# Performance work log

Measured on AMD Instinct MI355X. Metric: run time of the kernel, lower is better.

The kernel has to match this reference:

```python
import jax, jax.numpy as jnp
import numpy as np

B, S, D, H = 2, 2048, 512, 8
DH = D // H


def layer_norm(x, w, b, eps=1e-5):
    mu = x.mean(-1, keepdims=True)
    var = x.var(-1, keepdims=True)  # biased, matches nn.LayerNorm
    return (x - mu) / jnp.sqrt(var + eps) * w + b


def map_norm(qk, eps=1e-5):
    # torch.var default is unbiased (ddof=1)
    mu = qk.mean(-1, keepdims=True)
    var = qk.var(-1, ddof=1, keepdims=True)
    return (qk - mu) / jnp.sqrt(var + eps)


def sinmax(x):
    s = 1.0 + jnp.sin(10.0 * x)
    return s / s.sum(-1, keepdims=True)


def setup_inputs() -> dict:
    key = jax.random.key(0)
    ks = jax.random.split(key, 8)
    sc = 0.02
    return {
        "x": jax.random.normal(ks[0], (B, S, D), jnp.float32),
        "norm_w": jnp.ones((D,), jnp.float32),
        "norm_b": jnp.zeros((D,), jnp.float32),
        "qvk_w": jax.random.normal(ks[1], (D, 3 * D), jnp.float32) * sc,
        "qvk_b": jnp.zeros((3 * D,), jnp.float32),
        "concat_w": jax.random.normal(ks[2], (D, D), jnp.float32) * sc,
        "concat_b": jnp.zeros((D,), jnp.float32),
        "mlp_norm_w": jnp.ones((D,), jnp.float32),
        "mlp_norm_b": jnp.zeros((D,), jnp.float32),
        "mlp1_w": jax.random.normal(ks[3], (D, 2 * D), jnp.float32) * sc,
        "mlp1_b": jnp.zeros((2 * D,), jnp.float32),
        "mlp2_w": jax.random.normal(ks[4], (2 * D, D), jnp.float32) * sc,
        "mlp2_b": jnp.zeros((D,), jnp.float32),
    }


def reference(x, norm_w, norm_b, qvk_w, qvk_b, concat_w, concat_b,
              mlp_norm_w, mlp_norm_b, mlp1_w, mlp1_b, mlp2_w, mlp2_b):
    res = x
    xn = layer_norm(x, norm_w, norm_b)
    qvk = jax.nn.relu(xn @ qvk_w + qvk_b)                      # [B,S,3D]
    Q, K, V = qvk[..., :D], qvk[..., D:2 * D], qvk[..., 2 * D:]
    # contiguous d_per_head chunks per head == reshape to [B,S,H,DH]
    q = Q.reshape(B, S, H, DH).transpose(0, 2, 1, 3)           # [B,H,S,DH]
    k = K.reshape(B, S, H, DH).transpose(0, 2, 1, 3)
    v = V.reshape(B, S, H, DH).transpose(0, 2, 1, 3)
    qk = jnp.einsum('bhqd,bhkd->bhqk', q, k)                   # [B,H,S,S]
    qk = map_norm(qk)                                          # norm_ variant
    scores = sinmax(qk / np.sqrt(DH))                          # sinmax variant
    hv = jnp.einsum('bhqk,bhkd->bhqd', scores, v)
    attout = hv.transpose(0, 2, 1, 3).reshape(B, S, D)
    attout = attout @ concat_w + concat_b + res
    res_mlp = attout
    a = layer_norm(attout, mlp_norm_w, mlp_norm_b)
    h = jax.nn.gelu(a @ mlp1_w + mlp1_b, approximate=False)
    mlpout = h @ mlp2_w + mlp2_b
    return (mlpout + res_mlp, scores)
```

## Files before the change

### kernel.cpp

```cpp
#include <hip/hip_runtime.h>

#define Bb_ 2
#define S_ 2048
#define D_ 512
#define H_ 8
#define DH_ 64

typedef __attribute__((ext_vector_type(8))) __bf16 bf16x8;
typedef __attribute__((ext_vector_type(4))) __bf16 bf16x4;
typedef __attribute__((ext_vector_type(2))) __bf16 bf16x2;
typedef __attribute__((ext_vector_type(4))) float f32x4;
typedef __attribute__((ext_vector_type(8))) short short8;
typedef __attribute__((ext_vector_type(4))) unsigned u32x4;
typedef __attribute__((ext_vector_type(2))) unsigned u32x2;

__device__ __forceinline__ void gload_lds16(const void* g, void* l) {
  __builtin_amdgcn_global_load_lds(
      (const __attribute__((address_space(1))) unsigned int*)g,
      (__attribute__((address_space(3))) unsigned int*)l, 16, 0, 0);
}

__global__ __launch_bounds__(256) void wtrans_tile(
    const float* __restrict__ qvk_w, const float* __restrict__ concat_w,
    const float* __restrict__ mlp1_w, const float* __restrict__ mlp2_w,
    __bf16* __restrict__ qvk_wT, __bf16* __restrict__ concat_wT,
    __bf16* __restrict__ mlp1_wT, __bf16* __restrict__ mlp2_wT) {
  __shared__ __align__(16) __bf16 tl[64 * 72];
  int b = blockIdx.x;
  const float* w;
  __bf16* wt;
  int K, N, rel, TN;
  if (b < 192)      { w = qvk_w;    wt = qvk_wT;    K = 512;  N = 1536; rel = b;       TN = 24; }
  else if (b < 256) { w = concat_w; wt = concat_wT; K = 512;  N = 512;  rel = b - 192; TN = 8;  }
  else if (b < 384) { w = mlp1_w;   wt = mlp1_wT;   K = 512;  N = 1024; rel = b - 256; TN = 16; }
  else              { w = mlp2_w;   wt = mlp2_wT;   K = 1024; N = 512;  rel = b - 384; TN = 8;  }
  int tk = rel / TN, tn = rel % TN;
  int k0 = tk * 64, n0 = tn * 64;
  int t = threadIdx.x;
#pragma unroll
  for (int i = 0; i < 4; i++) {
    int idx = i * 256 + t;
    int kk = idx >> 4, c4 = idx & 15;
    float4 v = *reinterpret_cast<const float4*>(w + (long)(k0 + kk) * N + n0 + c4 * 4);
    int nb = c4 * 4;
    tl[(nb + 0) * 72 + kk] = (__bf16)v.x;
    tl[(nb + 1) * 72 + kk] = (__bf16)v.y;
    tl[(nb + 2) * 72 + kk] = (__bf16)v.z;
    tl[(nb + 3) * 72 + kk] = (__bf16)v.w;
  }
  __syncthreads();
#pragma unroll
  for (int i = 0; i < 2; i++) {
    int idx = i * 256 + t;
    int nn = idx >> 3, kc = idx & 7;
    bf16x8 vv = *reinterpret_cast<const bf16x8*>(&tl[nn * 72 + kc * 8]);
    *reinterpret_cast<bf16x8*>(wt + (long)(n0 + nn) * K + k0 + kc * 8) = vv;
  }
}

__global__ __launch_bounds__(256) void ln_kernel(const float* __restrict__ x,
                                                 const float* __restrict__ w,
                                                 const float* __restrict__ b,
                                                 __bf16* __restrict__ out) {
  long row = blockIdx.x;
  const float* xr = x + row * 512;
  int t = threadIdx.x;
  float2 v = *reinterpret_cast<const float2*>(xr + t * 2);
  float s = v.x + v.y;
  float sq = v.x * v.x + v.y * v.y;
#pragma unroll
  for (int m = 1; m < 64; m <<= 1) {
    s += __shfl_xor(s, m);
    sq += __shfl_xor(sq, m);
  }
  __shared__ float red[8];
  int wid = t >> 6;
  if ((t & 63) == 0) { red[wid] = s; red[wid + 4] = sq; }
  __syncthreads();
  s = red[0] + red[1] + red[2] + red[3];
  sq = red[4] + red[5] + red[6] + red[7];
  float mu = s * (1.f / 512.f);
  float var = sq * (1.f / 512.f) - mu * mu;
  float rs = rsqrtf(var + 1e-5f);
  int c = t * 2;
  float o0 = (v.x - mu) * rs * w[c] + b[c];
  float o1 = (v.y - mu) * rs * w[c + 1] + b[c + 1];
  bf16x2 ov;
  ov[0] = (__bf16)o0;
  ov[1] = (__bf16)o1;
  *reinterpret_cast<bf16x2*>(out + row * 512 + c) = ov;
}

template <int ACT, int OUTMODE, bool HASRES, int BM>
__global__ __launch_bounds__(256) void gemm_kernel(
    const __bf16* __restrict__ A, const __bf16* __restrict__ Bt,
    const float* __restrict__ bias, const float* __restrict__ res,
    float* __restrict__ outF, __bf16* __restrict__ outB,
    __bf16* __restrict__ outK, __bf16* __restrict__ outVt,
    int lda, int ldb, int ldc, int K) {
  __shared__ __align__(16) __bf16 smem[BM * 64 + 128 * 64];
  __bf16* As = smem;
  __bf16* Bs = smem + BM * 64;
  int t = threadIdx.x, lane = t & 63, wid = t >> 6;
  const __bf16* Ab = A + (long)blockIdx.y * BM * lda;
  const __bf16* Bb = Bt + (long)blockIdx.x * 128 * ldb;

  constexpr int WM = (BM == 128) ? 2 : 1;
  constexpr int FN = (BM == 128) ? 4 : 2;
  int wr = (WM == 2) ? (wid >> 1) : 0;
  int wc = (WM == 2) ? (wid & 1) : wid;
  int kq = lane >> 4;

  f32x4 acc[4][FN];
#pragma unroll
  for (int i = 0; i < 4; i++)
#pragma unroll
    for (int j = 0; j < FN; j++) acc[i][j] = (f32x4){0.f, 0.f, 0.f, 0.f};

  for (int k0 = 0; k0 < K; k0 += 64) {
    __syncthreads();
#pragma unroll
    for (int j = 0; j < BM / 32; j++) {
      int ci = wid * (BM * 2) + j * 64 + lane;
      int row = ci >> 3, c = ci & 7, sc = c ^ (row & 7);
      gload_lds16(Ab + (long)row * lda + k0 + sc * 8, &As[(wid * (BM * 2) + j * 64) * 8]);
    }
#pragma unroll
    for (int j = 0; j < 4; j++) {
      int ci = wid * 256 + j * 64 + lane;
      int row = ci >> 3, c = ci & 7, sc = c ^ (row & 7);
      gload_lds16(Bb + (long)row * ldb + k0 + sc * 8, &Bs[(wid * 256 + j * 64) * 8]);
    }
    __syncthreads();
#pragma unroll
    for (int ks = 0; ks < 2; ks++) {
      bf16x8 af[4], bfr[FN];
#pragma unroll
      for (int fm = 0; fm < 4; fm++) {
        int r = wr * 64 + fm * 16 + (lane & 15);
        int c = (ks * 4 + kq) ^ (r & 7);
        af[fm] = *reinterpret_cast<const bf16x8*>(&As[r * 64 + c * 8]);
      }
#pragma unroll
      for (int fn = 0; fn < FN; fn++) {
        int r = wc * (16 * FN) + fn * 16 + (lane & 15);
        int c = (ks * 4 + kq) ^ (r & 7);
        bfr[fn] = *reinterpret_cast<const bf16x8*>(&Bs[r * 64 + c * 8]);
      }
#pragma unroll
      for (int fm = 0; fm < 4; fm++)
#pragma unroll
        for (int fn = 0; fn < FN; fn++)
          acc[fm][fn] = __builtin_amdgcn_mfma_f32_16x16x32_bf16(af[fm], bfr[fn],
                                                                acc[fm][fn], 0, 0, 0);
    }
  }

  if constexpr (OUTMODE == 2) {
    __syncthreads();
    char* Cb = reinterpret_cast<char*>(smem);
#pragma unroll
    for (int fm = 0; fm < 4; fm++)
#pragma unroll
      for (int fn = 0; fn < FN; fn++) {
        int c = wc * 64 + fn * 16 + (lane & 15);
        int gcol = blockIdx.x * 128 + c;
        float bv = bias[gcol];
#pragma unroll
        for (int r4 = 0; r4 < 4; r4++) {
          int r = wr * 64 + fm * 16 + kq * 4 + r4;
          float v = fmaxf(acc[fm][fn][r4] + bv, 0.f);
          *reinterpret_cast<__bf16*>(Cb + r * 256 + (((c >> 3) ^ (r & 7)) << 4) +
                                     ((c & 7) << 1)) = (__bf16)v;
        }
      }
    __syncthreads();
    long bbq = (blockIdx.y * 128) >> 11;
    int srow0 = (blockIdx.y * 128) & 2047;
    if (blockIdx.x < 8) {
      int r = t >> 1, half = t & 1;
      int gcol = blockIdx.x * 128 + half * 64;
      __bf16* dst;
      if (gcol < 512)
        dst = outB + ((bbq * 8 + (gcol >> 6)) * 2048 + srow0 + r) * 64;
      else
        dst = outK + ((bbq * 8 + ((gcol - 512) >> 6)) * 2048 + srow0 + r) * 64;
      const char* srcrow = Cb + r * 256;
#pragma unroll
      for (int j = 0; j < 8; j++) {
        bf16x8 vv = *reinterpret_cast<const bf16x8*>(
            srcrow + ((((half * 8 + j) ^ (r & 7))) << 4));
        *reinterpret_cast<bf16x8*>(dst + j * 8) = vv;
      }
    } else {
      int d = t & 63, seg = t >> 6;
      int srow = srow0 + seg * 32;
#pragma unroll
      for (int h2 = 0; h2 < 2; h2++) {
        int c = h2 * 64 + d;
        int h = (blockIdx.x * 128 - 1024 + h2 * 64) >> 6;
        __bf16* dst = outVt + (bbq * 8 + h) * 131072 + (srow >> 5) * 2048 + d * 32;
        bf16x8 wv8[4];
#pragma unroll
        for (int i = 0; i < 32; i++) {
          int r = seg * 32 + i;
          __bf16 val = *reinterpret_cast<const __bf16*>(
              Cb + r * 256 + (((c >> 3) ^ (r & 7)) << 4) + ((c & 7) << 1));
          wv8[i >> 3][i & 7] = val;
        }
#pragma unroll
        for (int i4 = 0; i4 < 4; i4++)
          *reinterpret_cast<bf16x8*>(dst + i4 * 8) = wv8[i4];
      }
    }
    return;
  } else {
    long gr0 = (long)blockIdx.y * BM + wr * 64;
    long gc0 = (long)blockIdx.x * 128 + wc * (16 * FN);
#pragma unroll
    for (int fm = 0; fm < 4; fm++)
#pragma unroll
      for (int fn = 0; fn < FN; fn++) {
        int col = (int)gc0 + fn * 16 + (lane & 15);
        long rbase = gr0 + fm * 16 + kq * 4;
        float bv = bias ? bias[col] : 0.f;
#pragma unroll
        for (int r4 = 0; r4 < 4; r4++) {
          long grow = rbase + r4;
          float v = acc[fm][fn][r4] + bv;
          if (HASRES) v += res[grow * ldc + col];
          if (ACT == 1) v = fmaxf(v, 0.f);
          if (ACT == 2) v = 0.5f * v * (1.f + erff(v * 0.70710678118f));
          if (OUTMODE == 0) {
            outF[grow * ldc + col] = v;
          } else {
            outB[grow * ldc + col] = (__bf16)v;
          }
        }
      }
  }
}

__global__ __launch_bounds__(256) void gram_kernel(const __bf16* __restrict__ Kh,
                                                   float* __restrict__ gpart,
                                                   float* __restrict__ kpart) {
  int head = blockIdx.x >> 5, chunk = blockIdx.x & 31;
  __shared__ __align__(16) __bf16 kl[64 * 64];
  int t = threadIdx.x;
  const __bf16* src = Kh + ((long)head * 2048 + chunk * 64) * 64;
#pragma unroll
  for (int i = 0; i < 2; i++) {
    int e = (i * 256 + t) * 8;
    *reinterpret_cast<short8*>(&kl[e]) = *reinterpret_cast<const short8*>(&src[e]);
  }
  __syncthreads();
  int d1 = t & 63, g = t >> 6;
  float acc[16];
#pragma unroll
  for (int i = 0; i < 16; i++) acc[i] = 0.f;
  float kb = 0.f;
  for (int r = 0; r < 64; r++) {
    float k1 = (float)kl[r * 64 + d1];
    kb += k1;
    bf16x8 a = *reinterpret_cast<const bf16x8*>(&kl[r * 64 + g * 16]);
    bf16x8 b = *reinterpret_cast<const bf16x8*>(&kl[r * 64 + g * 16 + 8]);
#pragma unroll
    for (int i = 0; i < 8; i++) acc[i] += k1 * (float)a[i];
#pragma unroll
    for (int i = 0; i < 8; i++) acc[8 + i] += k1 * (float)b[i];
  }
  float* gp = gpart + ((long)chunk * 16 + head) * 4096 + d1 * 64 + g * 16;
#pragma unroll
  for (int i = 0; i < 16; i++) gp[i] = acc[i];
  if (g == 0) kpart[(chunk * 16 + head) * 64 + d1] = kb;
}

__global__ __launch_bounds__(256) void greduce_kernel(const float* __restrict__ gpart,
                                                      const float* __restrict__ kpart,
                                                      float* __restrict__ G,
                                                      float* __restrict__ kbar) {
  int idx = blockIdx.x * 256 + threadIdx.x;
  if (idx < 65536) {
    int head = idx >> 12, e = idx & 4095;
    float s = 0.f;
#pragma unroll 4
    for (int c = 0; c < 32; c++) s += gpart[((long)c * 16 + head) * 4096 + e];
    G[idx] = s;
  } else if (idx < 66560) {
    int k = idx - 65536;
    int head = k >> 6, d = k & 63;
    float s = 0.f;
#pragma unroll 4
    for (int c = 0; c < 32; c++) s += kpart[(c * 16 + head) * 64 + d];
    kbar[k] = s * (1.f / 2048.f);
  }
}

__global__ __launch_bounds__(256, 4) void stats_kernel(const __bf16* __restrict__ Qh,
                                                       const float* __restrict__ G,
                                                       const float* __restrict__ kbar,
                                                       float2* __restrict__ stats) {
  int head = blockIdx.x >> 5, sub = blockIdx.x & 31;
  __shared__ float Gl[4096];
  __shared__ float kbl[64];
  __shared__ __align__(16) float qlf[64 * 68];
  int t = threadIdx.x;
  const float* Gsrc = G + head * 4096;
#pragma unroll
  for (int i = 0; i < 4; i++) {
    int e = (i * 256 + t) * 4;
    *reinterpret_cast<float4*>(&Gl[e]) = *reinterpret_cast<const float4*>(&Gsrc[e]);
  }
  if (t < 16)
    *reinterpret_cast<float4*>(&kbl[t * 4]) =
        *reinterpret_cast<const float4*>(&kbar[head * 64 + t * 4]);
  const __bf16* qsrc = Qh + ((long)head * 2048 + sub * 64) * 64;
#pragma unroll
  for (int i = 0; i < 2; i++) {
    int e = (i * 256 + t) * 8;
    bf16x8 v = *reinterpret_cast<const bf16x8*>(&qsrc[e]);
    int row = e >> 6, col = e & 63;
    float* dst = &qlf[row * 68 + col];
#pragma unroll
    for (int j = 0; j < 8; j++) dst[j] = (float)v[j];
  }
  __syncthreads();
  int qrow = t >> 2, qt = t & 3;
  const float* qr = &qlf[qrow * 68];
  float mup = 0.f, s2p = 0.f;
#pragma unroll
  for (int i = 0; i < 16; i++) {
    int d1 = qt * 16 + i;
    const float* Gr = &Gl[d1 * 64];
    float acc = 0.f;
#pragma unroll
    for (int j = 0; j < 64; j++) acc += Gr[j] * qr[j];
    float q1 = qr[d1];
    s2p += q1 * acc;
    mup += q1 * kbl[d1];
  }
  mup += __shfl_xor(mup, 1); mup += __shfl_xor(mup, 2);
  s2p += __shfl_xor(s2p, 1); s2p += __shfl_xor(s2p, 2);
  if (qt == 0) {
    float mu = mup;
    float var = (s2p - 2048.f * mu * mu) * (1.f / 2047.f);
    stats[(head << 11) + sub * 64 + qrow] = make_float2(mu, rsqrtf(var + 1e-5f));
  }
}

__global__ __launch_bounds__(256) void attn6_kernel(
    const __bf16* __restrict__ Qh, const __bf16* __restrict__ Kh,
    const __bf16* __restrict__ Vp, const float2* __restrict__ stats,
    float* __restrict__ sco, __bf16* __restrict__ hv) {
  __shared__ __align__(16) __bf16 Ks[128 * 64];
  __shared__ __align__(16) __bf16 Vs[4 * 64 * 32];

  int bid = blockIdx.x;
  int xcd = bid & 7, j = bid >> 3;
  int head = xcd * 2 + (j >> 5);
  int qt = j & 31;
  int bb = head >> 3, hh = head & 7;
  int q0 = qt * 64;

  int t = threadIdx.x, lane = t & 63, wv = t >> 6;
  int cg = lane >> 4, ln = lane & 15;
  int sw7 = ln & 7, sw3 = ln & 3;

  int qrow = q0 + wv * 16 + ln;
  const __bf16* Qr = Qh + ((long)head * 2048 + qrow) * 64;
  bf16x8 qf0 = *reinterpret_cast<const bf16x8*>(Qr + cg * 8);
  bf16x8 qf1 = *reinterpret_cast<const bf16x8*>(Qr + 32 + cg * 8);
  float2 st = stats[(head << 11) + qrow];
  float mu = st.x, rs = st.y;

  const __bf16* Kbase = Kh + (long)head * 131072;
  const __bf16* Vbase = Vp + (long)head * 131072;

  float Z = 0.f;
  for (int kt = 0; kt < 16; kt++) {
    __syncthreads();
    const __bf16* Kt = Kbase + kt * 8192;
#pragma unroll
    for (int jj = 0; jj < 4; jj++) {
      int ci = wv * 256 + jj * 64 + lane;
      int row = ci >> 3, c = ci & 7, sc = c ^ (row & 7);
      gload_lds16(Kt + row * 64 + sc * 8, &Ks[(wv * 256 + jj * 64) * 8]);
    }
    __syncthreads();
#pragma unroll
    for (int sl = 0; sl < 8; sl++) {
      const __bf16* kr = &Ks[(sl * 16 + ln) * 64];
      bf16x8 a0 = *reinterpret_cast<const bf16x8*>(kr + ((cg ^ sw7) * 8));
      bf16x8 a1 = *reinterpret_cast<const bf16x8*>(kr + (((cg + 4) ^ sw7) * 8));
      f32x4 d = (f32x4){0.f, 0.f, 0.f, 0.f};
      d = __builtin_amdgcn_mfma_f32_16x16x32_bf16(a0, qf0, d, 0, 0, 0);
      d = __builtin_amdgcn_mfma_f32_16x16x32_bf16(a1, qf1, d, 0, 0, 0);
      Z += (1.f + __sinf(1.25f * (d[0] - mu) * rs));
      Z += (1.f + __sinf(1.25f * (d[1] - mu) * rs));
      Z += (1.f + __sinf(1.25f * (d[2] - mu) * rs));
      Z += (1.f + __sinf(1.25f * (d[3] - mu) * rs));
    }
  }
  Z += __shfl_xor(Z, 16);
  Z += __shfl_xor(Z, 32);
  float invZ = 1.f / Z;

  f32x4 hacc[4];
#pragma unroll
  for (int dt = 0; dt < 4; dt++) hacc[dt] = (f32x4){0.f, 0.f, 0.f, 0.f};
  float* srow = sco + ((long)head * 2048 + qrow) * 2048;

  for (int kt = 0; kt < 16; kt++) {
    __syncthreads();
    const __bf16* Kt = Kbase + kt * 8192;
    const __bf16* Vt = Vbase + kt * 8192;
#pragma unroll
    for (int jj = 0; jj < 4; jj++) {
      int ci = wv * 256 + jj * 64 + lane;
      int rowk = ci >> 3, ck = ci & 7, sck = ck ^ (rowk & 7);
      gload_lds16(Kt + rowk * 64 + sck * 8, &Ks[(wv * 256 + jj * 64) * 8]);
      int rowv = ci >> 2, cv = ci & 3, scv = cv ^ (rowv & 3);
      gload_lds16(Vt + rowv * 32 + scv * 8, &Vs[(wv * 256 + jj * 64) * 8]);
    }
    __syncthreads();
#pragma unroll
    for (int w = 0; w < 4; w++) {
      const __bf16* kr0 = &Ks[(w * 32 + ln) * 64];
      const __bf16* kr1 = &Ks[(w * 32 + 16 + ln) * 64];
      f32x4 d0 = (f32x4){0.f, 0.f, 0.f, 0.f}, d1 = (f32x4){0.f, 0.f, 0.f, 0.f};
      d0 = __builtin_amdgcn_mfma_f32_16x16x32_bf16(
          *reinterpret_cast<const bf16x8*>(kr0 + ((cg ^ sw7) * 8)), qf0, d0, 0, 0, 0);
      d0 = __builtin_amdgcn_mfma_f32_16x16x32_bf16(
          *reinterpret_cast<const bf16x8*>(kr0 + (((cg + 4) ^ sw7) * 8)), qf1, d0, 0, 0, 0);
      d1 = __builtin_amdgcn_mfma_f32_16x16x32_bf16(
          *reinterpret_cast<const bf16x8*>(kr1 + ((cg ^ sw7) * 8)), qf0, d1, 0, 0, 0);
      d1 = __builtin_amdgcn_mfma_f32_16x16x32_bf16(
          *reinterpret_cast<const bf16x8*>(kr1 + (((cg + 4) ^ sw7) * 8)), qf1, d1, 0, 0, 0);
      float p0 = 1.f + __sinf(1.25f * (d0[0] - mu) * rs);
      float p1 = 1.f + __sinf(1.25f * (d0[1] - mu) * rs);
      float p2 = 1.f + __sinf(1.25f * (d0[2] - mu) * rs);
      float p3 = 1.f + __sinf(1.25f * (d0[3] - mu) * rs);
      float p4 = 1.f + __sinf(1.25f * (d1[0] - mu) * rs);
      float p5 = 1.f + __sinf(1.25f * (d1[1] - mu) * rs);
      float p6 = 1.f + __sinf(1.25f * (d1[2] - mu) * rs);
      float p7 = 1.f + __sinf(1.25f * (d1[3] - mu) * rs);
      f32x4 o0 = (f32x4){p0 * invZ, p1 * invZ, p2 * invZ, p3 * invZ};
      f32x4 o1 = (f32x4){p4 * invZ, p5 * invZ, p6 * invZ, p7 * invZ};
      *reinterpret_cast<f32x4*>(srow + kt * 128 + w * 32 + cg * 4) = o0;
      *reinterpret_cast<f32x4*>(srow + kt * 128 + w * 32 + 16 + cg * 4) = o1;
      bf16x2 c0, c1, c2, c3;
      c0[0] = (__bf16)p0; c0[1] = (__bf16)p1;
      c1[0] = (__bf16)p2; c1[1] = (__bf16)p3;
      c2[0] = (__bf16)p4; c2[1] = (__bf16)p5;
      c3[0] = (__bf16)p6; c3[1] = (__bf16)p7;
      u32x4 pk = (u32x4){__builtin_bit_cast(unsigned, c0), __builtin_bit_cast(unsigned, c1),
                         __builtin_bit_cast(unsigned, c2), __builtin_bit_cast(unsigned, c3)};
      bf16x8 pf = __builtin_bit_cast(bf16x8, pk);
#pragma unroll
      for (int dt = 0; dt < 4; dt++) {
        const char* vr = reinterpret_cast<const char*>(Vs) + (w * 64 + dt * 16 + ln) * 64;
        int b0 = ((((cg >> 1) ^ sw3)) << 4) + ((cg & 1) << 3);
        int b1 = (((((cg >> 1) + 2) ^ sw3)) << 4) + ((cg & 1) << 3);
        u32x2 vlo = *reinterpret_cast<const u32x2*>(vr + b0);
        u32x2 vhi = *reinterpret_cast<const u32x2*>(vr + b1);
        u32x4 vpk = (u32x4){vlo[0], vlo[1], vhi[0], vhi[1]};
        bf16x8 vf = __builtin_bit_cast(bf16x8, vpk);
        hacc[dt] = __builtin_amdgcn_mfma_f32_16x16x32_bf16(vf, pf, hacc[dt], 0, 0, 0);
      }
    }
  }

  {
    __bf16* hq = hv + ((long)(bb * 2048) + qrow) * 512 + hh * 64;
#pragma unroll
    for (int dt = 0; dt < 4; dt++) {
      bf16x2 w0, w1;
      w0[0] = (__bf16)(hacc[dt][0] * invZ);
      w0[1] = (__bf16)(hacc[dt][1] * invZ);
      w1[0] = (__bf16)(hacc[dt][2] * invZ);
      w1[1] = (__bf16)(hacc[dt][3] * invZ);
      *reinterpret_cast<bf16x2*>(hq + dt * 16 + cg * 4) = w0;
      *reinterpret_cast<bf16x2*>(hq + dt * 16 + cg * 4 + 2) = w1;
    }
  }
}

extern "C" void kernel_launch(void* const* d_in, const int* in_sizes, int n_in,
                              void* d_out, int out_size, void* d_ws, size_t ws_size,
                              hipStream_t stream) {
  const float* x = (const float*)d_in[0];
  const float* norm_w = (const float*)d_in[1];
  const float* norm_b = (const float*)d_in[2];
  const float* qvk_w = (const float*)d_in[3];
  const float* qvk_b = (const float*)d_in[4];
  const float* concat_w = (const float*)d_in[5];
  const float* concat_b = (const float*)d_in[6];
  const float* mlp_norm_w = (const float*)d_in[7];
  const float* mlp_norm_b = (const float*)d_in[8];
  const float* mlp1_w = (const float*)d_in[9];
  const float* mlp1_b = (const float*)d_in[10];
  const float* mlp2_w = (const float*)d_in[11];
  const float* mlp2_b = (const float*)d_in[12];

  char* ws = (char*)d_ws;
  __bf16* qvk_wT = (__bf16*)(ws + 0);
  __bf16* concat_wT = (__bf16*)(ws + 1572864);
  __bf16* mlp1_wT = (__bf16*)(ws + 2097152);
  __bf16* mlp2_wT = (__bf16*)(ws + 3145728);
  __bf16* xn = (__bf16*)(ws + 4194304);
  __bf16* Qh = (__bf16*)(ws + 8388608);
  __bf16* Kh = (__bf16*)(ws + 12582912);
  __bf16* Vp = (__bf16*)(ws + 16777216);
  __bf16* hv = (__bf16*)(ws + 20971520);
  float* gpart = (float*)(ws + 25165824);
  float* attout = (float*)(ws + 25165824);
  float* kpart = (float*)(ws + 33554432);
  float* G = (float*)(ws + 33685504);
  float* kbar = (float*)(ws + 33947648);
  float2* stats = (float2*)(ws + 33951744);
  __bf16* a_b = (__bf16*)(ws + 33554432);
  __bf16* h_b = (__bf16*)(ws + 37748736);

  float* out0 = (float*)d_out;
  float* sco = out0 + 2097152;

  wtrans_tile<<<512, 256, 0, stream>>>(qvk_w, concat_w, mlp1_w, mlp2_w,
                                       qvk_wT, concat_wT, mlp1_wT, mlp2_wT);

  ln_kernel<<<4096, 256, 0, stream>>>(x, norm_w, norm_b, xn);

  gemm_kernel<1, 2, false, 128><<<dim3(12, 32), 256, 0, stream>>>(
      xn, qvk_wT, qvk_b, nullptr, nullptr, Qh, Kh, Vp, 512, 512, 1536, 512);

  gram_kernel<<<512, 256, 0, stream>>>(Kh, gpart, kpart);
  greduce_kernel<<<260, 256, 0, stream>>>(gpart, kpart, G, kbar);
  stats_kernel<<<512, 256, 0, stream>>>(Qh, G, kbar, stats);

  attn6_kernel<<<512, 256, 0, stream>>>(Qh, Kh, Vp, stats, sco, hv);

  gemm_kernel<0, 0, true, 64><<<dim3(4, 64), 256, 0, stream>>>(
      hv, concat_wT, concat_b, x, attout, nullptr, nullptr, nullptr, 512, 512, 512, 512);

  ln_kernel<<<4096, 256, 0, stream>>>(attout, mlp_norm_w, mlp_norm_b, a_b);

  gemm_kernel<2, 1, false, 64><<<dim3(8, 64), 256, 0, stream>>>(
      a_b, mlp1_wT, mlp1_b, nullptr, nullptr, h_b, nullptr, nullptr, 512, 512, 1024, 512);

  gemm_kernel<0, 0, true, 64><<<dim3(4, 64), 256, 0, stream>>>(
      h_b, mlp2_wT, mlp2_b, attout, out0, nullptr, nullptr, nullptr, 1024, 1024, 512, 1024);
}
```

Before: 199.5 us.

## Split attention key range across two wave groups and fuse weight prep with layernorm

The attention kernel now runs 512 threads per block: two groups of four waves each handle half of the key range for the same 64 query rows. Each group writes its own half of the score rows, and the groups combine their partial Z sums and hv accumulators through shared memory. This doubles the waves per block to hide the latency of the sin-heavy score work and LDS loads, at the cost of extra LDS, more barriers and a reduction at the end. Separately, the weight transpose and the first layernorm are merged into one launch, removing one kernel launch.

```diff
diff --git a/kernel.cpp b/kernel.cpp
--- a/kernel.cpp
+++ b/kernel.cpp
@@ -20,41 +20,72 @@
       (__attribute__((address_space(3))) unsigned int*)l, 16, 0, 0);
 }
 
-__global__ __launch_bounds__(256) void wtrans_tile(
+__global__ __launch_bounds__(256) void prep_kernel(
     const float* __restrict__ qvk_w, const float* __restrict__ concat_w,
     const float* __restrict__ mlp1_w, const float* __restrict__ mlp2_w,
     __bf16* __restrict__ qvk_wT, __bf16* __restrict__ concat_wT,
-    __bf16* __restrict__ mlp1_wT, __bf16* __restrict__ mlp2_wT) {
-  __shared__ __align__(16) __bf16 tl[64 * 72];
+    __bf16* __restrict__ mlp1_wT, __bf16* __restrict__ mlp2_wT,
+    const float* __restrict__ x, const float* __restrict__ norm_w,
+    const float* __restrict__ norm_b, __bf16* __restrict__ xn) {
   int b = blockIdx.x;
-  const float* w;
-  __bf16* wt;
-  int K, N, rel, TN;
-  if (b < 192)      { w = qvk_w;    wt = qvk_wT;    K = 512;  N = 1536; rel = b;       TN = 24; }
-  else if (b < 256) { w = concat_w; wt = concat_wT; K = 512;  N = 512;  rel = b - 192; TN = 8;  }
-  else if (b < 384) { w = mlp1_w;   wt = mlp1_wT;   K = 512;  N = 1024; rel = b - 256; TN = 16; }
-  else              { w = mlp2_w;   wt = mlp2_wT;   K = 1024; N = 512;  rel = b - 384; TN = 8;  }
-  int tk = rel / TN, tn = rel % TN;
-  int k0 = tk * 64, n0 = tn * 64;
   int t = threadIdx.x;
-#pragma unroll
-  for (int i = 0; i < 4; i++) {
-    int idx = i * 256 + t;
-    int kk = idx >> 4, c4 = idx & 15;
-    float4 v = *reinterpret_cast<const float4*>(w + (long)(k0 + kk) * N + n0 + c4 * 4);
-    int nb = c4 * 4;
-    tl[(nb + 0) * 72 + kk] = (__bf16)v.x;
-    tl[(nb + 1) * 72 + kk] = (__bf16)v.y;
-    tl[(nb + 2) * 72 + kk] = (__bf16)v.z;
-    tl[(nb + 3) * 72 + kk] = (__bf16)v.w;
-  }
-  __syncthreads();
-#pragma unroll
-  for (int i = 0; i < 2; i++) {
-    int idx = i * 256 + t;
-    int nn = idx >> 3, kc = idx & 7;
-    bf16x8 vv = *reinterpret_cast<const bf16x8*>(&tl[nn * 72 + kc * 8]);
-    *reinterpret_cast<bf16x8*>(wt + (long)(n0 + nn) * K + k0 + kc * 8) = vv;
+  if (b < 512) {
+    __shared__ __align__(16) __bf16 tl[64 * 72];
+    const float* w;
+    __bf16* wt;
+    int K, N, rel, TN;
+    if (b < 192)      { w = qvk_w;    wt = qvk_wT;    K = 512;  N = 1536; rel = b;       TN = 24; }
+    else if (b < 256) { w = concat_w; wt = concat_wT; K = 512;  N = 512;  rel = b - 192; TN = 8;  }
+    else if (b < 384) { w = mlp1_w;   wt = mlp1_wT;   K = 512;  N = 1024; rel = b - 256; TN = 16; }
+    else              { w = mlp2_w;   wt = mlp2_wT;   K = 1024; N = 512;  rel = b - 384; TN = 8;  }
+    int tk = rel / TN, tn = rel % TN;
+    int k0 = tk * 64, n0 = tn * 64;
+#pragma unroll
+    for (int i = 0; i < 4; i++) {
+      int idx = i * 256 + t;
+      int kk = idx >> 4, c4 = idx & 15;
+      float4 v = *reinterpret_cast<const float4*>(w + (long)(k0 + kk) * N + n0 + c4 * 4);
+      int nb = c4 * 4;
+      tl[(nb + 0) * 72 + kk] = (__bf16)v.x;
+      tl[(nb + 1) * 72 + kk] = (__bf16)v.y;
+      tl[(nb + 2) * 72 + kk] = (__bf16)v.z;
+      tl[(nb + 3) * 72 + kk] = (__bf16)v.w;
+    }
+    __syncthreads();
+#pragma unroll
+    for (int i = 0; i < 2; i++) {
+      int idx = i * 256 + t;
+      int nn = idx >> 3, kc = idx & 7;
+      bf16x8 vv = *reinterpret_cast<const bf16x8*>(&tl[nn * 72 + kc * 8]);
+      *reinterpret_cast<bf16x8*>(wt + (long)(n0 + nn) * K + k0 + kc * 8) = vv;
+    }
+  } else {
+    long row = b - 512;
+    const float* xr = x + row * 512;
+    float2 v = *reinterpret_cast<const float2*>(xr + t * 2);
+    float s = v.x + v.y;
+    float sq = v.x * v.x + v.y * v.y;
+#pragma unroll
+    for (int m = 1; m < 64; m <<= 1) {
+      s += __shfl_xor(s, m);
+      sq += __shfl_xor(sq, m);
+    }
+    __shared__ float red[8];
+    int wid = t >> 6;
+    if ((t & 63) == 0) { red[wid] = s; red[wid + 4] = sq; }
+    __syncthreads();
+    s = red[0] + red[1] + red[2] + red[3];
+    sq = red[4] + red[5] + red[6] + red[7];
+    float mu = s * (1.f / 512.f);
+    float var = sq * (1.f / 512.f) - mu * mu;
+    float rs = rsqrtf(var + 1e-5f);
+    int c = t * 2;
+    float o0 = (v.x - mu) * rs * norm_w[c] + norm_b[c];
+    float o1 = (v.y - mu) * rs * norm_w[c + 1] + norm_b[c + 1];
+    bf16x2 ov;
+    ov[0] = (__bf16)o0;
+    ov[1] = (__bf16)o1;
+    *reinterpret_cast<bf16x2*>(xn + row * 512 + c) = ov;
   }
 }
 
@@ -348,12 +379,14 @@
   }
 }
 
-__global__ __launch_bounds__(256) void attn6_kernel(
+__global__ __launch_bounds__(512, 4) void attn8_kernel(
     const __bf16* __restrict__ Qh, const __bf16* __restrict__ Kh,
     const __bf16* __restrict__ Vp, const float2* __restrict__ stats,
     float* __restrict__ sco, __bf16* __restrict__ hv) {
-  __shared__ __align__(16) __bf16 Ks[128 * 64];
-  __shared__ __align__(16) __bf16 Vs[4 * 64 * 32];
+  __shared__ __align__(16) __bf16 Ks[2][128 * 64];
+  __shared__ __align__(16) __bf16 Vs[2][4 * 64 * 32];
+  __shared__ float red2[8][16];
+  float* hvp = reinterpret_cast<float*>(Ks);
 
   int bid = blockIdx.x;
   int xcd = bid & 7, j = bid >> 3;
@@ -363,33 +396,34 @@
   int q0 = qt * 64;
 
   int t = threadIdx.x, lane = t & 63, wv = t >> 6;
+  int g = wv & 3, kh = wv >> 2;
   int cg = lane >> 4, ln = lane & 15;
   int sw7 = ln & 7, sw3 = ln & 3;
 
-  int qrow = q0 + wv * 16 + ln;
+  int qrow = q0 + g * 16 + ln;
   const __bf16* Qr = Qh + ((long)head * 2048 + qrow) * 64;
   bf16x8 qf0 = *reinterpret_cast<const bf16x8*>(Qr + cg * 8);
   bf16x8 qf1 = *reinterpret_cast<const bf16x8*>(Qr + 32 + cg * 8);
   float2 st = stats[(head << 11) + qrow];
   float mu = st.x, rs = st.y;
 
-  const __bf16* Kbase = Kh + (long)head * 131072;
-  const __bf16* Vbase = Vp + (long)head * 131072;
+  const __bf16* Kbase = Kh + (long)head * 131072 + kh * 65536;
+  const __bf16* Vbase = Vp + (long)head * 131072 + kh * 65536;
 
   float Z = 0.f;
-  for (int kt = 0; kt < 16; kt++) {
+  for (int kt = 0; kt < 8; kt++) {
     __syncthreads();
     const __bf16* Kt = Kbase + kt * 8192;
 #pragma unroll
     for (int jj = 0; jj < 4; jj++) {
-      int ci = wv * 256 + jj * 64 + lane;
+      int ci = g * 256 + jj * 64 + lane;
       int row = ci >> 3, c = ci & 7, sc = c ^ (row & 7);
-      gload_lds16(Kt + row * 64 + sc * 8, &Ks[(wv * 256 + jj * 64) * 8]);
+      gload_lds16(Kt + row * 64 + sc * 8, &Ks[kh][(g * 256 + jj * 64) * 8]);
     }
     __syncthreads();
 #pragma unroll
     for (int sl = 0; sl < 8; sl++) {
-      const __bf16* kr = &Ks[(sl * 16 + ln) * 64];
+      const __bf16* kr = &Ks[kh][(sl * 16 + ln) * 64];
       bf16x8 a0 = *reinterpret_cast<const bf16x8*>(kr + ((cg ^ sw7) * 8));
       bf16x8 a1 = *reinterpret_cast<const bf16x8*>(kr + (((cg + 4) ^ sw7) * 8));
       f32x4 d = (f32x4){0.f, 0.f, 0.f, 0.f};
@@ -403,30 +437,32 @@
   }
   Z += __shfl_xor(Z, 16);
   Z += __shfl_xor(Z, 32);
-  float invZ = 1.f / Z;
+  if (lane < 16) red2[wv][ln] = Z;
+  __syncthreads();
+  float invZ = 1.f / (red2[g][ln] + red2[g + 4][ln]);
 
   f32x4 hacc[4];
 #pragma unroll
   for (int dt = 0; dt < 4; dt++) hacc[dt] = (f32x4){0.f, 0.f, 0.f, 0.f};
-  float* srow = sco + ((long)head * 2048 + qrow) * 2048;
-
-  for (int kt = 0; kt < 16; kt++) {
+  float* srow = sco + ((long)head * 2048 + qrow) * 2048 + kh * 1024;
+
+  for (int kt = 0; kt < 8; kt++) {
     __syncthreads();
     const __bf16* Kt = Kbase + kt * 8192;
     const __bf16* Vt = Vbase + kt * 8192;
 #pragma unroll
     for (int jj = 0; jj < 4; jj++) {
-      int ci = wv * 256 + jj * 64 + lane;
+      int ci = g * 256 + jj * 64 + lane;
       int rowk = ci >> 3, ck = ci & 7, sck = ck ^ (rowk & 7);
-      gload_lds16(Kt + rowk * 64 + sck * 8, &Ks[(wv * 256 + jj * 64) * 8]);
+      gload_lds16(Kt + rowk * 64 + sck * 8, &Ks[kh][(g * 256 + jj * 64) * 8]);
       int rowv = ci >> 2, cv = ci & 3, scv = cv ^ (rowv & 3);
-      gload_lds16(Vt + rowv * 32 + scv * 8, &Vs[(wv * 256 + jj * 64) * 8]);
+      gload_lds16(Vt + rowv * 32 + scv * 8, &Vs[kh][(g * 256 + jj * 64) * 8]);
     }
     __syncthreads();
 #pragma unroll
     for (int w = 0; w < 4; w++) {
-      const __bf16* kr0 = &Ks[(w * 32 + ln) * 64];
-      const __bf16* kr1 = &Ks[(w * 32 + 16 + ln) * 64];
+      const __bf16* kr0 = &Ks[kh][(w * 32 + ln) * 64];
+      const __bf16* kr1 = &Ks[kh][(w * 32 + 16 + ln) * 64];
       f32x4 d0 = (f32x4){0.f, 0.f, 0.f, 0.f}, d1 = (f32x4){0.f, 0.f, 0.f, 0.f};
       d0 = __builtin_amdgcn_mfma_f32_16x16x32_bf16(
           *reinterpret_cast<const bf16x8*>(kr0 + ((cg ^ sw7) * 8)), qf0, d0, 0, 0, 0);
@@ -458,7 +494,7 @@
       bf16x8 pf = __builtin_bit_cast(bf16x8, pk);
 #pragma unroll
       for (int dt = 0; dt < 4; dt++) {
-        const char* vr = reinterpret_cast<const char*>(Vs) + (w * 64 + dt * 16 + ln) * 64;
+        const char* vr = reinterpret_cast<const char*>(Vs[kh]) + (w * 64 + dt * 16 + ln) * 64;
         int b0 = ((((cg >> 1) ^ sw3)) << 4) + ((cg & 1) << 3);
         int b1 = (((((cg >> 1) + 2) ^ sw3)) << 4) + ((cg & 1) << 3);
         u32x2 vlo = *reinterpret_cast<const u32x2*>(vr + b0);
@@ -470,15 +506,23 @@
     }
   }
 
-  {
+  __syncthreads();
+  if (kh == 1) {
+#pragma unroll
+    for (int dt = 0; dt < 4; dt++)
+      *reinterpret_cast<f32x4*>(hvp + ((g * 16 + ln) * 68 + dt * 16 + cg * 4)) = hacc[dt];
+  }
+  __syncthreads();
+  if (kh == 0) {
     __bf16* hq = hv + ((long)(bb * 2048) + qrow) * 512 + hh * 64;
 #pragma unroll
     for (int dt = 0; dt < 4; dt++) {
+      f32x4 o = *reinterpret_cast<const f32x4*>(hvp + ((g * 16 + ln) * 68 + dt * 16 + cg * 4));
       bf16x2 w0, w1;
-      w0[0] = (__bf16)(hacc[dt][0] * invZ);
-      w0[1] = (__bf16)(hacc[dt][1] * invZ);
-      w1[0] = (__bf16)(hacc[dt][2] * invZ);
-      w1[1] = (__bf16)(hacc[dt][3] * invZ);
+      w0[0] = (__bf16)((hacc[dt][0] + o[0]) * invZ);
+      w0[1] = (__bf16)((hacc[dt][1] + o[1]) * invZ);
+      w1[0] = (__bf16)((hacc[dt][2] + o[2]) * invZ);
+      w1[1] = (__bf16)((hacc[dt][3] + o[3]) * invZ);
       *reinterpret_cast<bf16x2*>(hq + dt * 16 + cg * 4) = w0;
       *reinterpret_cast<bf16x2*>(hq + dt * 16 + cg * 4 + 2) = w1;
     }
@@ -524,10 +568,9 @@
   float* out0 = (float*)d_out;
   float* sco = out0 + 2097152;
 
-  wtrans_tile<<<512, 256, 0, stream>>>(qvk_w, concat_w, mlp1_w, mlp2_w,
-                                       qvk_wT, concat_wT, mlp1_wT, mlp2_wT);
-
-  ln_kernel<<<4096, 256, 0, stream>>>(x, norm_w, norm_b, xn);
+  prep_kernel<<<4608, 256, 0, stream>>>(qvk_w, concat_w, mlp1_w, mlp2_w,
+                                        qvk_wT, concat_wT, mlp1_wT, mlp2_wT,
+                                        x, norm_w, norm_b, xn);
 
   gemm_kernel<1, 2, false, 128><<<dim3(12, 32), 256, 0, stream>>>(
       xn, qvk_wT, qvk_b, nullptr, nullptr, Qh, Kh, Vp, 512, 512, 1536, 512);
@@ -536,7 +579,7 @@
   greduce_kernel<<<260, 256, 0, stream>>>(gpart, kpart, G, kbar);
   stats_kernel<<<512, 256, 0, stream>>>(Qh, G, kbar, stats);
 
-  attn6_kernel<<<512, 256, 0, stream>>>(Qh, Kh, Vp, stats, sco, hv);
+  attn8_kernel<<<512, 512, 0, stream>>>(Qh, Kh, Vp, stats, sco, hv);
 
   gemm_kernel<0, 0, true, 64><<<dim3(4, 64), 256, 0, stream>>>(
       hv, concat_wT, concat_b, x, attout, nullptr, nullptr, nullptr, 512, 512, 512, 512);
```

Measured after the change: 195.1 us (median of 2 runs). 1.02x faster.
